# Optimization experiments

Hardware: AMD Instinct MI355X
Metric: run time of the kernel (lower is better)

The kernel has to match this reference:

```python
import jax, jax.numpy as jnp
import numpy as np

NUM_HEADS = 8
NUM_POINTS = 4


def _bilinear_gather(vl, loc, h, w):
    """MSDeformAttn bilinear sampling (align_corners=False, zero padding).
    vl: (BN, h*w, H, D) one level's values; loc: (BN, Q, H, P, 2) normalized [0,1].
    Returns (BN, Q, H, P, D)."""
    BN, _, H, D = vl.shape
    Q, P = loc.shape[1], loc.shape[3]
    x = loc[..., 0] * w - 0.5
    y = loc[..., 1] * h - 0.5
    x0 = jnp.floor(x); y0 = jnp.floor(y)
    lx = x - x0; ly = y - y0
    x0i = x0.astype(jnp.int32); y0i = y0.astype(jnp.int32)
    x1i = x0i + 1; y1i = y0i + 1
    vt = vl.transpose(0, 2, 1, 3)  # (BN, H, hw, D)

    def gather(yi, xi):
        valid = (yi >= 0) & (yi < h) & (xi >= 0) & (xi < w)
        idx = jnp.clip(yi, 0, h - 1) * w + jnp.clip(xi, 0, w - 1)  # (BN,Q,H,P)
        idx_t = idx.transpose(0, 2, 1, 3).reshape(BN, H, Q * P)
        g = jnp.take_along_axis(vt, idx_t[..., None], axis=2)  # (BN,H,QP,D)
        g = g.reshape(BN, H, Q, P, D).transpose(0, 2, 1, 3, 4)
        return jnp.where(valid[..., None], g, jnp.zeros((), vl.dtype))

    w00 = ((1 - ly) * (1 - lx))[..., None]
    w01 = ((1 - ly) * lx)[..., None]
    w10 = (ly * (1 - lx))[..., None]
    w11 = (ly * lx)[..., None]
    return (gather(y0i, x0i) * w00 + gather(y0i, x1i) * w01
            + gather(y1i, x0i) * w10 + gather(y1i, x1i) * w11)


def _forward(query, value, reference_points, query_mask, spatial_shapes, level_start_index,
             Wv, bv, Woff, boff, Watt, batt, Wo, bo):
    B, Z, Y, X, C = query.shape
    Q = Z * Y * X
    BN = value.shape[0]
    N = BN // B  # cameras per sample (uniform lengths)
    H, P = NUM_HEADS, NUM_POINTS
    shapes = np.asarray(spatial_shapes)  # static level shapes
    starts = np.asarray(level_start_index)
    L = shapes.shape[0]
    D = C // H
    mask = query_mask.astype(query.dtype)  # (BN, Q)
    # expand each sample's voxel queries to its N cameras
    qf = jnp.broadcast_to(query.reshape(B, 1, Q, C), (B, N, Q, C)).reshape(BN, Q, C)
    v = (value @ Wv + bv).reshape(BN, -1, H, D)
    off = (qf @ Woff + boff).reshape(BN, Q, H, L, P, 2)
    aw = jax.nn.softmax((qf @ Watt + batt).reshape(BN, Q, H, L * P), axis=-1)
    aw = aw.reshape(BN, Q, H, L, P)
    # offset_normalizer = (w, h) per level
    normalizer = jnp.asarray(np.stack([shapes[:, 1], shapes[:, 0]], -1), query.dtype)
    loc = reference_points[:, :, None, None, None, :] + off / normalizer[None, None, None, :, None, :]
    out = jnp.zeros((BN, Q, H, D), query.dtype)
    for l in range(L):
        h, w = int(shapes[l, 0]), int(shapes[l, 1])
        s = int(starts[l])
        vl = v[:, s:s + h * w]
        sampled = _bilinear_gather(vl, loc[:, :, :, l], h, w)  # (BN,Q,H,P,D)
        out = out + jnp.einsum('bqhpd,bqhp->bqhd', sampled, aw[:, :, :, l])
    attn = out.reshape(BN, Q, C) @ Wo + bo
    # identity + attn, then rebatch_mask_sequence zeroes non-masked voxels
    full = (qf + attn) * mask[..., None]
    summed = full.reshape(B, N, Q, C).sum(axis=1)
    counts = jnp.maximum(mask.reshape(B, N, Q).sum(axis=1), 1.0)
    return (summed / counts[..., None]).reshape(B, Z, Y, X, C)


def setup_inputs() -> dict:
    key = jax.random.key(0)
    ks = jax.random.split(key, 9)
    B, N = 2, 4
    Z, Y, X, C = 8, 32, 32, 256
    Q = Z * Y * X
    BN = B * N
    shapes = np.array([[64, 112], [32, 56], [16, 28], [8, 14]], np.int64)
    starts = np.concatenate([[0], np.cumsum(shapes[:, 0] * shapes[:, 1])[:-1]]).astype(np.int64)
    Nv = int((shapes[:, 0] * shapes[:, 1]).sum())  # 9520
    H, L, P = NUM_HEADS, shapes.shape[0], NUM_POINTS
    s = 0.02
    return dict(
        query=jax.random.normal(ks[0], (B, Z, Y, X, C), jnp.float32),
        value=jax.random.normal(ks[1], (BN, Nv, C), jnp.float32),
        reference_points=jax.random.uniform(ks[2], (BN, Q, 2), jnp.float32),
        query_mask=jax.random.bernoulli(ks[3], 0.6, (BN, Q)),
        spatial_shapes=jnp.asarray(shapes),
        level_start_index=jnp.asarray(starts),
        Wv=jax.random.normal(ks[4], (C, C), jnp.float32) * s,
        bv=jnp.zeros((C,), jnp.float32),
        Woff=jax.random.normal(ks[5], (C, H * L * P * 2), jnp.float32) * s,
        boff=jax.random.normal(ks[6], (H * L * P * 2,), jnp.float32),
        Watt=jax.random.normal(ks[7], (C, H * L * P), jnp.float32) * s,
        batt=jnp.zeros((H * L * P,), jnp.float32),
        Wo=jax.random.normal(ks[8], (C, C), jnp.float32) * s,
        bo=jnp.zeros((C,), jnp.float32),
    )


def reference(query, value, reference_points, query_mask, spatial_shapes, level_start_index,
              Wv, bv, Woff, boff, Watt, batt, Wo, bo):
    return _forward(query, value, reference_points, query_mask, spatial_shapes, level_start_index,
                    Wv, bv, Woff, boff, Watt, batt, Wo, bo)
```

## Files before the change

### kernel.cpp

```cpp
#include <hip/hip_runtime.h>
#include <cstdint>
#include <cstddef>

#define QQ 8192
#define CDIM 256
#define NV 9520
#define NLVL 4
#define NPTS 4
#define NHEAD 8

typedef __attribute__((ext_vector_type(8))) short short8;
typedef __attribute__((ext_vector_type(4))) float f32x4;
typedef __attribute__((ext_vector_type(2))) float f32x2;

__device__ __forceinline__ unsigned short f2bf(float f)
{
    unsigned u = __float_as_uint(f);
    unsigned r = (u + 0x7fffu + ((u >> 16) & 1u)) >> 16;
    return (unsigned short)r;
}
__device__ __forceinline__ unsigned pk2bf(float a, float b)
{
    return (unsigned)f2bf(a) | ((unsigned)f2bf(b) << 16);
}
__device__ __forceinline__ float bf2f(unsigned short u)
{
    return __uint_as_float(((unsigned)u) << 16);
}

__global__ void pack_weights_detect_kernel(
    const float* __restrict__ Wv,
    const float* __restrict__ Woff, const float* __restrict__ boff,
    const float* __restrict__ Watt, const float* __restrict__ batt,
    const float* __restrict__ Wo,
    const unsigned int* __restrict__ maskw,
    unsigned short* __restrict__ Wt_v,
    unsigned short* __restrict__ Wt_oa,
    unsigned short* __restrict__ Wt_o,
    float* __restrict__ bias_oa,
    int* __restrict__ flag)
{
    const int n = blockIdx.x, k = threadIdx.x;
    if (n < 256) {
        Wt_v[n * 256 + k] = f2bf(Wv[(size_t)k * 256 + n]);
    } else if (n < 512) {
        const int c = n - 256;
        Wt_oa[c * 256 + k] = f2bf(Woff[(size_t)k * 256 + c]);
        if (k == 0) bias_oa[c] = boff[c];
    } else if (n < 640) {
        const int c = n - 512;
        Wt_oa[(256 + c) * 256 + k] = f2bf(Watt[(size_t)k * 128 + c]);
        if (k == 0) bias_oa[256 + c] = batt[c];
    } else if (n < 768) {
        const int c = n - 640;
        Wt_oa[(384 + c) * 256 + k] = 0;
        if (k == 0) bias_oa[384 + c] = 0.f;
    } else if (n < 1024) {
        const int c = n - 768;
        Wt_o[c * 256 + k] = f2bf(Wo[(size_t)k * 256 + c]);
    } else {
        __shared__ int notI32, notF32;
        if (k == 0) { notI32 = 0; notF32 = 0; }
        __syncthreads();
        for (int i = k; i < 1024; i += 256) {
            unsigned v = maskw[i];
            if (v > 1u) notI32 = 1;
            if (v != 0u && v != 0x3F800000u) notF32 = 1;
        }
        __syncthreads();
        if (k == 0) *flag = (!notI32) ? 1 : ((!notF32) ? 2 : 0);
    }
}

__global__ __launch_bounds__(512) void mega_gemm_kernel(
    const float* __restrict__ value, const float* __restrict__ query,
    const unsigned short* __restrict__ Wt_v,
    const unsigned short* __restrict__ Wt_oa,
    const float* __restrict__ bv, const float* __restrict__ bias_oa,
    unsigned short* __restrict__ v_proj, unsigned short* __restrict__ offatt)
{
    __shared__ unsigned short As[128 * 64];
    __shared__ unsigned short Bs[256 * 64];
    const int bid = blockIdx.x;
    int role, m0;
    const float* A;
    const unsigned short* Bt;
    if (bid < 595)      { role = 0; m0 = bid * 128;         A = value; Bt = Wt_v; }
    else if (bid < 723) { role = 1; m0 = (bid - 595) * 128; A = query; Bt = Wt_oa; }
    else                { role = 2; m0 = (bid - 723) * 128; A = query; Bt = Wt_oa + 256 * 256; }

    const int tid  = threadIdx.x;
    const int lane = tid & 63;
    const int wave = tid >> 6;
    const int wm = wave >> 2, wn = wave & 3;
    const int lr = lane & 15, g = lane >> 4;

    f32x4 acc[4][4];
    #pragma unroll
    for (int mi = 0; mi < 4; ++mi)
        #pragma unroll
        for (int ni = 0; ni < 4; ++ni)
            acc[mi][ni] = (f32x4){0.f, 0.f, 0.f, 0.f};

    for (int kt = 0; kt < 4; ++kt) {
        uint4 ra[2], rb[4];
        #pragma unroll
        for (int it = 0; it < 2; ++it) {
            const int fb  = it * 512 + tid;
            const int row = fb >> 3, kb = fb & 7;
            const float* p = A + (size_t)(m0 + row) * 256 + kt * 64 + kb * 8;
            float4 f0 = *(const float4*)p;
            float4 f1 = *(const float4*)(p + 4);
            ra[it] = make_uint4(pk2bf(f0.x, f0.y), pk2bf(f0.z, f0.w),
                                pk2bf(f1.x, f1.y), pk2bf(f1.z, f1.w));
        }
        #pragma unroll
        for (int it = 0; it < 4; ++it) {
            const int fb  = it * 512 + tid;
            const int row = fb >> 3, kb = fb & 7;
            rb[it] = *(const uint4*)(Bt + (size_t)row * 256 + kt * 64 + kb * 8);
        }
        __syncthreads();
        #pragma unroll
        for (int it = 0; it < 2; ++it) {
            const int fb  = it * 512 + tid;
            const int row = fb >> 3, kb = fb & 7;
            *(uint4*)&As[row * 64 + ((kb ^ (row & 7)) << 3)] = ra[it];
        }
        #pragma unroll
        for (int it = 0; it < 4; ++it) {
            const int fb  = it * 512 + tid;
            const int row = fb >> 3, kb = fb & 7;
            *(uint4*)&Bs[row * 64 + ((kb ^ (row & 7)) << 3)] = rb[it];
        }
        __syncthreads();
        #pragma unroll
        for (int kk = 0; kk < 2; ++kk) {
            const int kb = kk * 4 + g;
            short8 af[4], bf[4];
            #pragma unroll
            for (int mi = 0; mi < 4; ++mi) {
                const int row = wm * 64 + mi * 16 + lr;
                af[mi] = *(const short8*)&As[row * 64 + ((kb ^ (row & 7)) << 3)];
            }
            #pragma unroll
            for (int ni = 0; ni < 4; ++ni) {
                const int row = wn * 64 + ni * 16 + lr;
                bf[ni] = *(const short8*)&Bs[row * 64 + ((kb ^ (row & 7)) << 3)];
            }
            #pragma unroll
            for (int mi = 0; mi < 4; ++mi)
                #pragma unroll
                for (int ni = 0; ni < 4; ++ni)
                    acc[mi][ni] = __builtin_amdgcn_mfma_f32_16x16x32_bf16(
                        af[mi], bf[ni], acc[mi][ni], 0, 0, 0);
        }
    }

    float bcol[4];
    #pragma unroll
    for (int ni = 0; ni < 4; ++ni) {
        const int gn = wn * 64 + ni * 16 + lr;
        bcol[ni] = (role == 0) ? bv[gn]
                 : (role == 1) ? bias_oa[gn] : bias_oa[256 + gn];
    }
    if (role == 0) {
        #pragma unroll
        for (int half = 0; half < 2; ++half) {
            __syncthreads();
            if ((wn >> 1) == half) {
                const int wc = wn & 1;
                #pragma unroll
                for (int mi = 0; mi < 4; ++mi)
                    #pragma unroll
                    for (int j = 0; j < 4; ++j) {
                        const int r = wm * 64 + mi * 16 + g * 4 + j;
                        #pragma unroll
                        for (int ni = 0; ni < 4; ++ni) {
                            const int col = wc * 64 + ni * 16 + lr;
                            Bs[r * 128 + col] = f2bf(acc[mi][ni][j] + bcol[ni]);
                        }
                    }
            }
            __syncthreads();
            #pragma unroll
            for (int i = 0; i < 4; ++i) {
                const int f = i * 512 + tid;
                const int r = f >> 4, c16 = f & 15;
                *(uint4*)(v_proj + (size_t)(m0 + r) * 256 + half * 128 + c16 * 8) =
                    *(const uint4*)&Bs[r * 128 + c16 * 8];
            }
        }
    } else {
        #pragma unroll
        for (int mi = 0; mi < 4; ++mi) {
            #pragma unroll
            for (int j = 0; j < 4; ++j) {
                const int gm = m0 + wm * 64 + mi * 16 + g * 4 + j;
                #pragma unroll
                for (int ni = 0; ni < 4; ++ni) {
                    const int gn = wn * 64 + ni * 16 + lr;
                    const float r = acc[mi][ni][j] + bcol[ni];
                    if (role == 1)
                        offatt[(size_t)gm * 384 + gn] = f2bf(r);
                    else if (gn < 128)
                        offatt[(size_t)gm * 384 + 256 + gn] = f2bf(r);
                }
            }
        }
    }
}

__global__ __launch_bounds__(256) void wo_final_kernel(
    const unsigned short* __restrict__ S,
    const unsigned short* __restrict__ Wt_o,
    const float* __restrict__ query,
    const float* __restrict__ bo,
    const float* __restrict__ cnts,
    float* __restrict__ out)
{
    __shared__ unsigned short As[64 * 64];
    __shared__ unsigned short Bs[256 * 64];
    const int tid  = threadIdx.x;
    const int lane = tid & 63;
    const int wn   = tid >> 6;
    const int lr = lane & 15, g = lane >> 4;
    const int m0 = blockIdx.x * 64;

    f32x4 acc[4][4];
    #pragma unroll
    for (int mi = 0; mi < 4; ++mi)
        #pragma unroll
        for (int ni = 0; ni < 4; ++ni)
            acc[mi][ni] = (f32x4){0.f, 0.f, 0.f, 0.f};

    for (int kt = 0; kt < 4; ++kt) {
        uint4 ra[2], rb[8];
        #pragma unroll
        for (int it = 0; it < 2; ++it) {
            const int fb  = it * 256 + tid;
            const int row = fb >> 3, kb = fb & 7;
            ra[it] = *(const uint4*)(S + (size_t)(m0 + row) * 256 + kt * 64 + kb * 8);
        }
        #pragma unroll
        for (int it = 0; it < 8; ++it) {
            const int fb  = it * 256 + tid;
            const int row = fb >> 3, kb = fb & 7;
            rb[it] = *(const uint4*)(Wt_o + (size_t)row * 256 + kt * 64 + kb * 8);
        }
        __syncthreads();
        #pragma unroll
        for (int it = 0; it < 2; ++it) {
            const int fb  = it * 256 + tid;
            const int row = fb >> 3, kb = fb & 7;
            *(uint4*)&As[row * 64 + ((kb ^ (row & 7)) << 3)] = ra[it];
        }
        #pragma unroll
        for (int it = 0; it < 8; ++it) {
            const int fb  = it * 256 + tid;
            const int row = fb >> 3, kb = fb & 7;
            *(uint4*)&Bs[row * 64 + ((kb ^ (row & 7)) << 3)] = rb[it];
        }
        __syncthreads();
        #pragma unroll
        for (int kk = 0; kk < 2; ++kk) {
            const int kb = kk * 4 + g;
            short8 af[4], bf[4];
            #pragma unroll
            for (int mi = 0; mi < 4; ++mi) {
                const int row = mi * 16 + lr;
                af[mi] = *(const short8*)&As[row * 64 + ((kb ^ (row & 7)) << 3)];
            }
            #pragma unroll
            for (int ni = 0; ni < 4; ++ni) {
                const int row = wn * 64 + ni * 16 + lr;
                bf[ni] = *(const short8*)&Bs[row * 64 + ((kb ^ (row & 7)) << 3)];
            }
            #pragma unroll
            for (int mi = 0; mi < 4; ++mi)
                #pragma unroll
                for (int ni = 0; ni < 4; ++ni)
                    acc[mi][ni] = __builtin_amdgcn_mfma_f32_16x16x32_bf16(
                        af[mi], bf[ni], acc[mi][ni], 0, 0, 0);
        }
    }

    float bcol[4];
    #pragma unroll
    for (int ni = 0; ni < 4; ++ni)
        bcol[ni] = bo[wn * 64 + ni * 16 + lr];
    #pragma unroll
    for (int mi = 0; mi < 4; ++mi) {
        #pragma unroll
        for (int j = 0; j < 4; ++j) {
            const int gm = m0 + mi * 16 + g * 4 + j;
            const float sm = cnts[gm];
            const float inv = 1.f / fmaxf(sm, 1.f);
            #pragma unroll
            for (int ni = 0; ni < 4; ++ni) {
                const int gn = wn * 64 + ni * 16 + lr;
                const float qv = query[(size_t)gm * CDIM + gn] + bcol[ni];
                out[(size_t)gm * CDIM + gn] = (sm * qv + acc[mi][ni][j]) * inv;
            }
        }
    }
}

__device__ __forceinline__ float read_mask(const void* p, int f, size_t i)
{
    if (f == 1) return (float)((const int*)p)[i];
    if (f == 2) return ((const float*)p)[i];
    return (float)((const unsigned char*)p)[i];
}

__global__ __launch_bounds__(256) void sample_reduce_kernel(
    const unsigned short* __restrict__ v,
    const unsigned short* __restrict__ offatt,
    const float* __restrict__ refp,
    const void* __restrict__ maskp,
    const int* __restrict__ flag,
    unsigned short* __restrict__ S,
    float* __restrict__ cnts)
{
    __shared__ int4   sidx[4][NHEAD][17];
    __shared__ float4 swt[4][NHEAD][17];
    __shared__ float  red[4][CDIM];
    __shared__ float  smv[4];
    const int tid  = threadIdx.x;
    const int wn   = tid >> 6;
    const int lane = tid & 63;
    const int bq   = blockIdx.x;
    const int b    = bq >> 13;
    const int q    = bq & (QQ - 1);
    const int bn   = b * 4 + wn;

    const float mn = read_mask(maskp, *flag, (size_t)bn * QQ + q);
    if (lane == 0) smv[wn] = mn;

    const unsigned short* oa = offatt + (size_t)bq * 384;
    const float rx = refp[((size_t)bn * QQ + q) * 2 + 0];
    const float ry = refp[((size_t)bn * QQ + q) * 2 + 1];

    #pragma unroll
    for (int cc = 0; cc < 2; ++cc) {
        const int c = lane + cc * 64;
        const int hcomb = c >> 4;
        const int pcomb = c & 15;
        const int l = (c >> 2) & 3;
        const int hh = 64 >> l;
        const int ww = 112 >> l;
        const int s  = (l > 0 ? 7168 : 0) + (l > 1 ? 1792 : 0) + (l > 2 ? 448 : 0);
        const unsigned offxy = *(const unsigned*)(oa + c * 2);
        const float offx = __uint_as_float(offxy << 16);
        const float offy = __uint_as_float(offxy & 0xffff0000u);
        const float logit = bf2f(oa[256 + c]);
        float mx = logit;
        #pragma unroll
        for (int d = 1; d < 16; d <<= 1) mx = fmaxf(mx, __shfl_xor(mx, d));
        const float e = __expf(logit - mx);
        float se = e;
        #pragma unroll
        for (int d = 1; d < 16; d <<= 1) se += __shfl_xor(se, d);
        const float aw = e / se;

        const float x = rx * (float)ww - 0.5f + offx;
        const float y = ry * (float)hh - 0.5f + offy;
        const float x0f = floorf(x), y0f = floorf(y);
        const float lx = x - x0f, ly = y - y0f;
        const int x0 = (int)x0f, y0 = (int)y0f;
        const int x1 = x0 + 1,  y1 = y0 + 1;
        const bool vx0 = (x0 >= 0) & (x0 < ww);
        const bool vx1 = (x1 >= 0) & (x1 < ww);
        const bool vy0 = (y0 >= 0) & (y0 < hh);
        const bool vy1 = (y1 >= 0) & (y1 < hh);
        const int xc0 = min(max(x0, 0), ww - 1);
        const int xc1 = min(max(x1, 0), ww - 1);
        const int yc0 = min(max(y0, 0), hh - 1);
        const int yc1 = min(max(y1, 0), hh - 1);
        float w00 = (1.f - ly) * (1.f - lx) * aw;
        float w01 = (1.f - ly) * lx * aw;
        float w10 = ly * (1.f - lx) * aw;
        float w11 = ly * lx * aw;
        w00 = (vy0 & vx0) ? w00 : 0.f;
        w01 = (vy0 & vx1) ? w01 : 0.f;
        w10 = (vy1 & vx0) ? w10 : 0.f;
        w11 = (vy1 & vx1) ? w11 : 0.f;
        sidx[wn][hcomb][pcomb] = make_int4(s + yc0 * ww + xc0, s + yc0 * ww + xc1,
                                           s + yc1 * ww + xc0, s + yc1 * ww + xc1);
        swt[wn][hcomb][pcomb]  = make_float4(w00, w01, w10, w11);
    }

    f32x2 c01[4], c23[4];
    #pragma unroll
    for (int k = 0; k < 4; ++k) { c01[k] = (f32x2){0.f, 0.f}; c23[k] = (f32x2){0.f, 0.f}; }
    if (mn != 0.f) {
        const int h  = lane >> 3;
        const int d4 = lane & 7;
        const int laneoff = h * 8 + d4;
        const unsigned long long* vb =
            (const unsigned long long*)(v + (size_t)bn * NV * CDIM);
        #pragma unroll
        for (int pb = 0; pb < 4; ++pb) {
            unsigned long long gld[16];
            float4 wts[4];
            #pragma unroll
            for (int j = 0; j < 4; ++j) {
                const int p = pb * 4 + j;
                const int4 id = sidx[wn][h][p];
                wts[j] = swt[wn][h][p];
                gld[j * 4 + 0] = vb[(size_t)(id.x * 64 + laneoff)];
                gld[j * 4 + 1] = vb[(size_t)(id.y * 64 + laneoff)];
                gld[j * 4 + 2] = vb[(size_t)(id.z * 64 + laneoff)];
                gld[j * 4 + 3] = vb[(size_t)(id.w * 64 + laneoff)];
            }
            asm volatile("" ::
                "v"(gld[0]),  "v"(gld[1]),  "v"(gld[2]),  "v"(gld[3]),
                "v"(gld[4]),  "v"(gld[5]),  "v"(gld[6]),  "v"(gld[7]),
                "v"(gld[8]),  "v"(gld[9]),  "v"(gld[10]), "v"(gld[11]),
                "v"(gld[12]), "v"(gld[13]), "v"(gld[14]), "v"(gld[15]));
            #pragma unroll
            for (int j = 0; j < 4; ++j) {
                const float4 wt = wts[j];
                const float wa[4] = {wt.x, wt.y, wt.z, wt.w};
                #pragma unroll
                for (int cidx = 0; cidx < 4; ++cidx) {
                    const unsigned long long gg = gld[j * 4 + cidx];
                    const unsigned glo = (unsigned)gg;
                    const unsigned ghi = (unsigned)(gg >> 32);
                    const f32x2 wv = (f32x2){wa[cidx], wa[cidx]};
                    #define BFLO(u) __uint_as_float((u) << 16)
                    #define BFHI(u) __uint_as_float((u) & 0xffff0000u)
                    c01[cidx] += wv * (f32x2){BFLO(glo), BFHI(glo)};
                    c23[cidx] += wv * (f32x2){BFLO(ghi), BFHI(ghi)};
                    #undef BFLO
                    #undef BFHI
                }
            }
        }
    }
    const f32x2 acc01 = (c01[0] + c01[1]) + (c01[2] + c01[3]);
    const f32x2 acc23 = (c23[0] + c23[1]) + (c23[2] + c23[3]);
    *(float4*)&red[wn][lane * 4] =
        make_float4(acc01.x, acc01.y, acc23.x, acc23.y);
    __syncthreads();

    const float ssum = red[0][tid] + red[1][tid] + red[2][tid] + red[3][tid];
    S[(size_t)bq * CDIM + tid] = f2bf(ssum);
    if (tid == 0) cnts[bq] = smv[0] + smv[1] + smv[2] + smv[3];
}

extern "C" void kernel_launch(void* const* d_in, const int* in_sizes, int n_in,
                              void* d_out, int out_size, void* d_ws, size_t ws_size,
                              hipStream_t stream)
{
    (void)in_sizes; (void)n_in; (void)out_size; (void)ws_size;
    const float* query = (const float*)d_in[0];
    const float* value = (const float*)d_in[1];
    const float* refp  = (const float*)d_in[2];
    const void*  maskp = d_in[3];
    const float* Wv    = (const float*)d_in[6];
    const float* bv    = (const float*)d_in[7];
    const float* Woff  = (const float*)d_in[8];
    const float* boff  = (const float*)d_in[9];
    const float* Watt  = (const float*)d_in[10];
    const float* batt  = (const float*)d_in[11];
    const float* Wo    = (const float*)d_in[12];
    const float* bo    = (const float*)d_in[13];
    float* out = (float*)d_out;
    char* ws = (char*)d_ws;

    unsigned short* v_proj  = (unsigned short*)(ws + 0);
    unsigned short* offatt  = (unsigned short*)(ws + 38993920);
    unsigned short* S_bf16  = (unsigned short*)(ws + 51576832);
    unsigned short* Wt_v    = (unsigned short*)(ws + 59965440);
    unsigned short* Wt_oa   = (unsigned short*)(ws + 60096512);
    unsigned short* Wt_o    = (unsigned short*)(ws + 60358656);
    float*          bias_oa = (float*)(ws + 60489728);
    float*          cnts    = (float*)(ws + 60491776);
    int*            flag    = (int*)(ws + 60557312);

    pack_weights_detect_kernel<<<1025, 256, 0, stream>>>(
        Wv, Woff, boff, Watt, batt, Wo, (const unsigned int*)maskp,
        Wt_v, Wt_oa, Wt_o, bias_oa, flag);

    mega_gemm_kernel<<<851, 512, 0, stream>>>(
        value, query, Wt_v, Wt_oa, bv, bias_oa, v_proj, offatt);

    sample_reduce_kernel<<<16384, 256, 0, stream>>>(
        v_proj, offatt, refp, maskp, flag, S_bf16, cnts);

    wo_final_kernel<<<256, 256, 0, stream>>>(
        S_bf16, Wt_o, query, bo, cnts, out);
}
```

Before: 200.3 us.

## Store projected values head-major so bilinear gathers read per-head contiguous rows

The value projection epilogue now writes v_proj in a (BN, head, pixel, 32) layout instead of (BN, pixel, 256). The sampling kernel indexes each head's plane directly, so a head's 8 lanes read a contiguous 64-byte row per corner. This is meant to improve cache and locality behaviour of the scattered gathers. The empty asm barrier that forced all gathers to be issued before use is also removed, which leaves load scheduling to the compiler. The store side now does an integer division per element and writes 64-byte chunks instead of 256-byte rows.

```diff
diff --git a/kernel.cpp b/kernel.cpp
--- a/kernel.cpp
+++ b/kernel.cpp
@@ -185,10 +185,17 @@
             __syncthreads();
             #pragma unroll
             for (int i = 0; i < 4; ++i) {
-                const int f = i * 512 + tid;
-                const int r = f >> 4, c16 = f & 15;
-                *(uint4*)(v_proj + (size_t)(m0 + r) * 256 + half * 128 + c16 * 8) =
-                    *(const uint4*)&Bs[r * 128 + c16 * 8];
+                const int u  = i * 512 + tid;
+                const int hl = u >> 9;
+                const int r  = (u >> 2) & 127;
+                const int c4 = u & 3;
+                const int rowg = m0 + r;
+                const unsigned bnq = (unsigned)rowg / 9520u;
+                const int pix = rowg - (int)bnq * 9520;
+                const int hgl = half * 4 + hl;
+                unsigned short* dst = v_proj +
+                    (((size_t)(bnq * 8 + hgl) * 9520 + pix) << 5) + c4 * 8;
+                *(uint4*)dst = *(const uint4*)&Bs[r * 128 + hl * 32 + c4 * 8];
             }
         }
     } else {
@@ -396,9 +403,8 @@
     if (mn != 0.f) {
         const int h  = lane >> 3;
         const int d4 = lane & 7;
-        const int laneoff = h * 8 + d4;
-        const unsigned long long* vb =
-            (const unsigned long long*)(v + (size_t)bn * NV * CDIM);
+        const unsigned long long* vb = (const unsigned long long*)v
+            + (size_t)bn * (NHEAD * NV * 8) + (size_t)h * (NV * 8) + d4;
         #pragma unroll
         for (int pb = 0; pb < 4; ++pb) {
             unsigned long long gld[16];
@@ -408,16 +414,11 @@
                 const int p = pb * 4 + j;
                 const int4 id = sidx[wn][h][p];
                 wts[j] = swt[wn][h][p];
-                gld[j * 4 + 0] = vb[(size_t)(id.x * 64 + laneoff)];
-                gld[j * 4 + 1] = vb[(size_t)(id.y * 64 + laneoff)];
-                gld[j * 4 + 2] = vb[(size_t)(id.z * 64 + laneoff)];
-                gld[j * 4 + 3] = vb[(size_t)(id.w * 64 + laneoff)];
-            }
-            asm volatile("" ::
-                "v"(gld[0]),  "v"(gld[1]),  "v"(gld[2]),  "v"(gld[3]),
-                "v"(gld[4]),  "v"(gld[5]),  "v"(gld[6]),  "v"(gld[7]),
-                "v"(gld[8]),  "v"(gld[9]),  "v"(gld[10]), "v"(gld[11]),
-                "v"(gld[12]), "v"(gld[13]), "v"(gld[14]), "v"(gld[15]));
+                gld[j * 4 + 0] = vb[(size_t)id.x * 8];
+                gld[j * 4 + 1] = vb[(size_t)id.y * 8];
+                gld[j * 4 + 2] = vb[(size_t)id.z * 8];
+                gld[j * 4 + 3] = vb[(size_t)id.w * 8];
+            }
             #pragma unroll
             for (int j = 0; j < 4; ++j) {
                 const float4 wt = wts[j];
@@ -440,7 +441,7 @@
     }
     const f32x2 acc01 = (c01[0] + c01[1]) + (c01[2] + c01[3]);
     const f32x2 acc23 = (c23[0] + c23[1]) + (c23[2] + c23[3]);
-    *(float4*)&red[wn][lane * 4] =
+    *(float4*)&red[wn][(lane >> 3) * 32 + (lane & 7) * 4] =
         make_float4(acc01.x, acc01.y, acc23.x, acc23.y);
     __syncthreads();
 
```

After: 191.8 us. -4.2%, faster.
